# Performance work log

Measured on AMD Instinct MI355X. Metric: run time of the kernel, lower is better.

Reference implementation:

```python
import jax, jax.numpy as jnp
import numpy as np

BATCH = 32768
NUM_CLASSES = 1024  # balanced binary hierarchy => 10 levels, 1023 internal nodes


def setup_inputs() -> dict:
    key = jax.random.key(0)
    outputs = jax.random.normal(key, (BATCH, NUM_CLASSES), dtype=jnp.float32)
    return {"outputs": outputs}


def reference(outputs) -> jnp.ndarray:
    """SoftEmbeddedDecisionRules.forward for a balanced binary hierarchy.

    For every internal node: child logit = mean of raw logits over the child's
    leaf (class) set, softmax over the node's children, then multiply each
    class's running probability by the prob of the branch containing it.
    With a balanced binary tree over C classes, level l has 2^l nodes, each
    child covering a contiguous block of C / 2^(l+1) classes, so the per-node
    Python loop of the original collapses into one reshape+mean+softmax per
    level (log2(C) fused passes total).
    """
    B, C = outputs.shape
    depth = C.bit_length() - 1  # log2(C), static
    class_probs = jnp.ones((B, C), dtype=outputs.dtype)
    for level in range(depth):
        n_nodes = 1 << level
        seg = C // (2 * n_nodes)  # classes per child subtree
        # node logits: mean of raw logits over each child's class block
        node_logits = outputs.reshape(B, n_nodes, 2, seg).mean(axis=-1)  # [B, n, 2]
        probs = jax.nn.softmax(node_logits, axis=-1)  # softmax over children
        # scatter-multiply child prob onto every class in that child's subtree
        expanded = jnp.broadcast_to(probs[..., None], (B, n_nodes, 2, seg)).reshape(B, C)
        class_probs = class_probs * expanded
    return class_probs
```

## Files before the change

kernel.cpp:

```cpp
#include <hip/hip_runtime.h>


#define C 1024

__device__ __forceinline__ float sigmoid_of(float x) {
    return __builtin_amdgcn_rcpf(1.0f + __expf(x));
}

__global__ __launch_bounds__(256) void hier_softmax_kernel(
    const float* __restrict__ in, float* __restrict__ out) {
    __shared__ float wsum[4];

    const int row = blockIdx.x;
    const int tid = threadIdx.x;
    const int wave = tid >> 6;
    const int lane = tid & 63;

    const float4 v = ((const float4*)(in + (size_t)row * C))[tid];

    const float s2a = v.x + v.y;
    const float s2b = v.z + v.w;
    float sum = s2a + s2b;

    const float pA = sigmoid_of(v.y - v.x);
    const float pB = sigmoid_of(v.w - v.z);
    const float p9 = sigmoid_of((s2b - s2a) * 0.5f);

    float common = 1.0f;
    float inv_seg = 0.25f;
#pragma unroll
    for (int k = 1; k <= 32; k <<= 1) {
        const float partner = __shfl_xor(sum, k, 64);
        common *= sigmoid_of((partner - sum) * inv_seg);
        sum += partner;
        inv_seg *= 0.5f;
    }

    if (lane == 0) wsum[wave] = sum;
    __syncthreads();

    const float partnerW = wsum[wave ^ 1];
    common *= sigmoid_of((partnerW - sum) * (1.0f / 256.0f));
    const float myHalf = sum + partnerW;
    const float otherHalf = wsum[wave ^ 2] + wsum[wave ^ 3];
    common *= sigmoid_of((otherHalf - myHalf) * (1.0f / 512.0f));

    const float cl = common * p9;
    const float cr = common - cl;
    float4 o;
    o.x = cl * pA;
    o.y = cl - o.x;
    o.z = cr * pB;
    o.w = cr - o.z;
    ((float4*)(out + (size_t)row * C))[tid] = o;
}

extern "C" void kernel_launch(void* const* d_in, const int* in_sizes, int n_in,
                              void* d_out, int out_size, void* d_ws, size_t ws_size,
                              hipStream_t stream) {
    const float* in = (const float*)d_in[0];
    float* out = (float*)d_out;
    const int B = in_sizes[0] / C;
    hier_softmax_kernel<<<B, 256, 0, stream>>>(in, out);
}
```

Baseline: 216.5 us.

## Map one row per wavefront with 16 elements per lane, dropping shared memory sync

Each 64-lane wave now handles a whole 1024-float row, with each lane loading four float4s (16 contiguous values). The lowest four tree levels are resolved in registers and the upper six through wave shuffles. This removes the LDS exchange and __syncthreads between waves, and the grid shrinks to B/4 blocks. The trade-off is more registers per thread and strided per-lane accesses (each lane covers 64 contiguous bytes), which may coalesce less well than the previous consecutive float4 per thread.

```diff
diff --git a/kernel.cpp b/kernel.cpp
--- a/kernel.cpp
+++ b/kernel.cpp
@@ -9,25 +9,38 @@
 
 __global__ __launch_bounds__(256) void hier_softmax_kernel(
     const float* __restrict__ in, float* __restrict__ out) {
-    __shared__ float wsum[4];
+    const int tid  = threadIdx.x;
+    const int lane = tid & 63;
+    const int wave = tid >> 6;
+    const int row  = (blockIdx.x << 2) + wave;
 
-    const int row = blockIdx.x;
-    const int tid = threadIdx.x;
-    const int wave = tid >> 6;
-    const int lane = tid & 63;
+    const float4* src = (const float4*)(in + (size_t)row * C + lane * 16);
+    const float4 a = src[0], b = src[1], c = src[2], d = src[3];
 
-    const float4 v = ((const float4*)(in + (size_t)row * C))[tid];
+    const float v[16] = {a.x, a.y, a.z, a.w, b.x, b.y, b.z, b.w,
+                         c.x, c.y, c.z, c.w, d.x, d.y, d.z, d.w};
 
-    const float s2a = v.x + v.y;
-    const float s2b = v.z + v.w;
-    float sum = s2a + s2b;
-
-    const float pA = sigmoid_of(v.y - v.x);
-    const float pB = sigmoid_of(v.w - v.z);
-    const float p9 = sigmoid_of((s2b - s2a) * 0.5f);
+    float s2[8], s4[4], s8[2], p1[8], p2[4], p4[2];
+#pragma unroll
+    for (int i = 0; i < 8; ++i) {
+        s2[i] = v[2 * i] + v[2 * i + 1];
+        p1[i] = sigmoid_of(v[2 * i + 1] - v[2 * i]);
+    }
+#pragma unroll
+    for (int i = 0; i < 4; ++i) {
+        s4[i] = s2[2 * i] + s2[2 * i + 1];
+        p2[i] = sigmoid_of((s2[2 * i + 1] - s2[2 * i]) * 0.5f);
+    }
+#pragma unroll
+    for (int i = 0; i < 2; ++i) {
+        s8[i] = s4[2 * i] + s4[2 * i + 1];
+        p4[i] = sigmoid_of((s4[2 * i + 1] - s4[2 * i]) * 0.25f);
+    }
+    const float p8 = sigmoid_of((s8[1] - s8[0]) * 0.125f);
+    float sum = s8[0] + s8[1];
 
     float common = 1.0f;
-    float inv_seg = 0.25f;
+    float inv_seg = 1.0f / 16.0f;
 #pragma unroll
     for (int k = 1; k <= 32; k <<= 1) {
         const float partner = __shfl_xor(sum, k, 64);
@@ -36,23 +49,28 @@
         inv_seg *= 0.5f;
     }
 
-    if (lane == 0) wsum[wave] = sum;
-    __syncthreads();
+    const float t8L = common * p8, t8R = common - t8L;
+    float t4[4];
+    t4[0] = t8L * p4[0]; t4[1] = t8L - t4[0];
+    t4[2] = t8R * p4[1]; t4[3] = t8R - t4[2];
+    float t2[8];
+#pragma unroll
+    for (int i = 0; i < 4; ++i) {
+        t2[2 * i]     = t4[i] * p2[i];
+        t2[2 * i + 1] = t4[i] - t2[2 * i];
+    }
+    float o[16];
+#pragma unroll
+    for (int i = 0; i < 8; ++i) {
+        o[2 * i]     = t2[i] * p1[i];
+        o[2 * i + 1] = t2[i] - o[2 * i];
+    }
 
-    const float partnerW = wsum[wave ^ 1];
-    common *= sigmoid_of((partnerW - sum) * (1.0f / 256.0f));
-    const float myHalf = sum + partnerW;
-    const float otherHalf = wsum[wave ^ 2] + wsum[wave ^ 3];
-    common *= sigmoid_of((otherHalf - myHalf) * (1.0f / 512.0f));
-
-    const float cl = common * p9;
-    const float cr = common - cl;
-    float4 o;
-    o.x = cl * pA;
-    o.y = cl - o.x;
-    o.z = cr * pB;
-    o.w = cr - o.z;
-    ((float4*)(out + (size_t)row * C))[tid] = o;
+    float4* dst = (float4*)(out + (size_t)row * C + lane * 16);
+    dst[0] = make_float4(o[0],  o[1],  o[2],  o[3]);
+    dst[1] = make_float4(o[4],  o[5],  o[6],  o[7]);
+    dst[2] = make_float4(o[8],  o[9],  o[10], o[11]);
+    dst[3] = make_float4(o[12], o[13], o[14], o[15]);
 }
 
 extern "C" void kernel_launch(void* const* d_in, const int* in_sizes, int n_in,
@@ -61,5 +79,5 @@
     const float* in = (const float*)d_in[0];
     float* out = (float*)d_out;
     const int B = in_sizes[0] / C;
-    hier_softmax_kernel<<<B, 256, 0, stream>>>(in, out);
+    hier_softmax_kernel<<<B / 4, 256, 0, stream>>>(in, out);
 }
```

Result: slower. 232.9 us (+7.6%).

## Process one row per wavefront to eliminate shared memory and block barrier

Applied to the files above, without the earlier changes.

Each wavefront now handles a whole row, with every lane loading four float4 chunks, instead of a 256-thread block sharing one row. The top two tree levels are computed in registers from the four per-chunk sums, so the shared-memory exchange and __syncthreads go away. The grid shrinks by four. The trade-off is more registers per thread and more independent shuffles per step.

```diff
diff --git a/kernel.cpp b/kernel.cpp
--- a/kernel.cpp
+++ b/kernel.cpp
@@ -9,50 +9,66 @@
 
 __global__ __launch_bounds__(256) void hier_softmax_kernel(
     const float* __restrict__ in, float* __restrict__ out) {
-    __shared__ float wsum[4];
+    const int tid  = threadIdx.x;
+    const int lane = tid & 63;
+    const int wave = tid >> 6;
+    const int row  = (blockIdx.x << 2) + wave;
 
-    const int row = blockIdx.x;
-    const int tid = threadIdx.x;
-    const int wave = tid >> 6;
-    const int lane = tid & 63;
+    const float* rowp = in + (size_t)row * C;
 
-    const float4 v = ((const float4*)(in + (size_t)row * C))[tid];
+    float4 L[4];
+    L[0] = ((const float4*)(rowp +   0))[lane];
+    L[1] = ((const float4*)(rowp + 256))[lane];
+    L[2] = ((const float4*)(rowp + 512))[lane];
+    L[3] = ((const float4*)(rowp + 768))[lane];
 
-    const float s2a = v.x + v.y;
-    const float s2b = v.z + v.w;
-    float sum = s2a + s2b;
+    float pA[4], pB[4], p2[4], sum[4], com[4];
+#pragma unroll
+    for (int q = 0; q < 4; ++q) {
+        const float s2a = L[q].x + L[q].y;
+        const float s2b = L[q].z + L[q].w;
+        pA[q]  = sigmoid_of(L[q].y - L[q].x);
+        pB[q]  = sigmoid_of(L[q].w - L[q].z);
+        p2[q]  = sigmoid_of((s2b - s2a) * 0.5f);
+        sum[q] = s2a + s2b;
+        com[q] = 1.0f;
+    }
 
-    const float pA = sigmoid_of(v.y - v.x);
-    const float pB = sigmoid_of(v.w - v.z);
-    const float p9 = sigmoid_of((s2b - s2a) * 0.5f);
-
-    float common = 1.0f;
     float inv_seg = 0.25f;
 #pragma unroll
     for (int k = 1; k <= 32; k <<= 1) {
-        const float partner = __shfl_xor(sum, k, 64);
-        common *= sigmoid_of((partner - sum) * inv_seg);
-        sum += partner;
+        float pr[4];
+#pragma unroll
+        for (int q = 0; q < 4; ++q) pr[q] = __shfl_xor(sum[q], k, 64);
+#pragma unroll
+        for (int q = 0; q < 4; ++q) {
+            com[q] *= sigmoid_of((pr[q] - sum[q]) * inv_seg);
+            sum[q] += pr[q];
+        }
         inv_seg *= 0.5f;
     }
 
-    if (lane == 0) wsum[wave] = sum;
-    __syncthreads();
+    const float pRoot = sigmoid_of((sum[2] + sum[3] - sum[0] - sum[1]) * (1.0f / 512.0f));
+    const float pL    = sigmoid_of((sum[1] - sum[0]) * (1.0f / 256.0f));
+    const float pR    = sigmoid_of((sum[3] - sum[2]) * (1.0f / 256.0f));
+    float t[4];
+    t[0] = pRoot * pL;          t[1] = pRoot - t[0];
+    const float rRoot = 1.0f - pRoot;
+    t[2] = rRoot * pR;          t[3] = rRoot - t[2];
 
-    const float partnerW = wsum[wave ^ 1];
-    common *= sigmoid_of((partnerW - sum) * (1.0f / 256.0f));
-    const float myHalf = sum + partnerW;
-    const float otherHalf = wsum[wave ^ 2] + wsum[wave ^ 3];
-    common *= sigmoid_of((otherHalf - myHalf) * (1.0f / 512.0f));
-
-    const float cl = common * p9;
-    const float cr = common - cl;
-    float4 o;
-    o.x = cl * pA;
-    o.y = cl - o.x;
-    o.z = cr * pB;
-    o.w = cr - o.z;
-    ((float4*)(out + (size_t)row * C))[tid] = o;
+    float* orow = out + (size_t)row * C;
+#pragma unroll
+    for (int q = 0; q < 4; ++q) {
+        const float base = t[q] * com[q];
+        const float cl = base * p2[q];
+        const float cr = base - cl;
+        float4 o;
+        o.x = cl * pA[q];
+        o.y = cl - o.x;
+        o.z = cr * pB[q];
+        o.w = cr - o.z;
+        ((float4*)(orow + q * 256))[lane] = o;
+    }
 }
 
 extern "C" void kernel_launch(void* const* d_in, const int* in_sizes, int n_in,
@@ -61,5 +77,5 @@
     const float* in = (const float*)d_in[0];
     float* out = (float*)d_out;
     const int B = in_sizes[0] / C;
-    hier_softmax_kernel<<<B, 256, 0, stream>>>(in, out);
+    hier_softmax_kernel<<<B / 4, 256, 0, stream>>>(in, out);
 }
```

After: 228.1 us. 1.05x slower.
